# Kernel optimization log

Measured on AMD Instinct MI355X. Metric: run time of the kernel, lower is better.

The kernel has to match this reference:

```python
import jax, jax.numpy as jnp
import numpy as np

B, T, D, H = 128, 256, 64, 512
MISSING = 128.0  # MISSING_VALUE marker from AJ-RNN repo


def _lstm_params(key, in_dim):
    k1, k2 = jax.random.split(key)
    K = jax.random.normal(k1, (in_dim, 4 * H), jnp.float32) * 0.05
    R = jax.random.normal(k2, (H, 4 * H), jnp.float32) * 0.05
    # Keras LSTMCell: zeros bias with unit forget bias (gate order i, f, c, o)
    b = jnp.concatenate([jnp.zeros((H,)), jnp.ones((H,)), jnp.zeros((2 * H,))]).astype(jnp.float32)
    return K, R, b


def setup_inputs() -> dict:
    key = jax.random.key(0)
    ks = jax.random.split(key, 6)
    x = jax.random.normal(ks[0], (B, T, D), jnp.float32)
    miss = jax.random.uniform(ks[1], (B, T, D)) < 0.2
    x = jnp.where(miss, MISSING, x)  # inject missing-value markers
    k0, r0, b0 = _lstm_params(ks[2], D)   # layer 0: input dim D
    k1, r1, b1 = _lstm_params(ks[3], H)   # layer 1: input dim H
    W = jax.random.normal(ks[4], (H, D), jnp.float32) * 0.1  # imputation kernel
    bias = jnp.full((D,), 0.1, jnp.float32)
    return dict(x=x, k0=k0, r0=r0, b0=b0, k1=k1, r1=r1, b1=b1, W=W, bias=bias)


def _lstm_cell(x, h, c, K, R, b):
    z = x @ K + h @ R + b  # [B, 4H]
    i, f, g, o = jnp.split(z, 4, axis=-1)
    i = jax.nn.sigmoid(i)
    f = jax.nn.sigmoid(f)
    g = jnp.tanh(g)
    o = jax.nn.sigmoid(o)
    c_new = f * c + i * g
    h_new = o * jnp.tanh(c_new)
    return h_new, c_new


def reference(x, k0, r0, b0, k1, r1, b1, W, bias):
    xs = jnp.swapaxes(x, 0, 1)          # [T, B, D]
    flags = jnp.arange(T) > 0           # t==0 uses raw input, no imputation

    def step(carry, inp):
        h1, c1, h2, c2 = carry
        x_t, flag = inp
        pred = h2 @ W + bias            # prediction from previous top-layer output
        cur = jnp.where(flag & (x_t == MISSING), pred, x_t)
        h1, c1 = _lstm_cell(cur, h1, c1, k0, r0, b0)
        h2, c2 = _lstm_cell(h1, h2, c2, k1, r1, b1)
        return (h1, c1, h2, c2), h2

    init = tuple(jnp.zeros((B, H), jnp.float32) for _ in range(4))
    _, outs = jax.lax.scan(step, init, (xs, flags))  # outs: [T, B, H]

    # tf.concat(outputs[:-1], axis=1) then reshape [-1, H] == batch-major, time inner
    hidden = jnp.swapaxes(outs[:-1], 0, 1).reshape(-1, H)  # [B*(T-1), H]
    prediction = hidden @ W + bias                          # [B*(T-1), D]
    last_cell = outs[-1]                                    # [B, H]
    return prediction, last_cell
```

## Files before the change

### kernel.cpp

```cpp
#include <hip/hip_runtime.h>
#include <hip/hip_bf16.h>


typedef __bf16        v8bf  __attribute__((ext_vector_type(8)));
typedef float         f32x4 __attribute__((ext_vector_type(4)));
typedef unsigned int  u32x4 __attribute__((ext_vector_type(4)));

constexpr int B_ = 128, T_ = 256, D_ = 64, H_ = 512;

constexpr size_t OFF_WP1 = 0;
constexpr size_t OFF_WP2 = 2359296;
constexpr size_t OFF_WPP = 6553600;
constexpr size_t OFF_H1G = 6619136;
constexpr size_t OFF_H2G = 6750208;
constexpr size_t OFF_FLG = 6881280;

__device__ __forceinline__ v8bf ldv(const __hip_bfloat16* p) {
  return *reinterpret_cast<const v8bf*>(p);
}
__device__ __forceinline__ float sigf(float x) { return 1.0f / (1.0f + __expf(-x)); }
__device__ __forceinline__ float tanhfast(float x) {
  x = fminf(15.0f, fmaxf(-15.0f, x));
  float e = __expf(-2.0f * x);
  return (1.0f - e) / (1.0f + e);
}

__device__ __forceinline__ void st_llc_u16(void* p, unsigned v) {
  asm volatile("global_store_short %0, %1, off sc0 sc1" :: "v"(p), "v"(v) : "memory");
}

__device__ __forceinline__ void ld_llc64(const char* g, u32x4& a, u32x4& b,
                                         u32x4& c, u32x4& d) {
  asm volatile(
      "global_load_dwordx4 %0, %4, off sc0 sc1\n\t"
      "global_load_dwordx4 %1, %4, off offset:16 sc0 sc1\n\t"
      "global_load_dwordx4 %2, %4, off offset:32 sc0 sc1\n\t"
      "global_load_dwordx4 %3, %4, off offset:48 sc0 sc1\n\t"
      "s_waitcnt vmcnt(0)"
      : "=&v"(a), "=&v"(b), "=&v"(c), "=&v"(d)
      : "v"(g)
      : "memory");
}

__device__ __forceinline__ void stage_tile(const __hip_bfloat16* gsrc,
                                           __hip_bfloat16 (*tile)[512], int tid) {
  const int row = tid >> 4;
  const int o0  = (tid & 15) * 64;
  const char* g = (const char*)gsrc + row * 1024 + o0;
  char* lb = (char*)(&tile[row][0]);
  const int sw = (row & 7) << 4;
  u32x4 a, b, c, d;
  ld_llc64(g, a, b, c, d);
  *(u32x4*)(lb + ((o0 +  0) ^ sw)) = a;
  *(u32x4*)(lb + ((o0 + 16) ^ sw)) = b;
  *(u32x4*)(lb + ((o0 + 32) ^ sw)) = c;
  *(u32x4*)(lb + ((o0 + 48) ^ sw)) = d;
}

__global__ __launch_bounds__(256) void pack_weights(
    const float* __restrict__ kp, const float* __restrict__ rp,
    int krows, int ncols, int nkc, int nct, __hip_bfloat16* __restrict__ out) {
  int tid = blockIdx.x * 256 + threadIdx.x;
  int total = nct * nkc * 64;
  if (tid >= total) return;
  int L  = tid & 63;
  int kc = (tid >> 6) % nkc;
  int ct = tid / (64 * nkc);
  int n  = ct * 16 + (L & 15);
  int kb = kc * 32 + (L >> 4) * 8;
  __hip_bfloat16* dst = out + (size_t)tid * 8;
#pragma unroll
  for (int j = 0; j < 8; ++j) {
    int kk = kb + j;
    float v = (kk < krows) ? kp[kk * ncols + n] : rp[(kk - krows) * ncols + n];
    dst[j] = __float2bfloat16(v);
  }
}

__global__ __launch_bounds__(256) void init_state(
    __hip_bfloat16* __restrict__ h1g, __hip_bfloat16* __restrict__ h2g,
    unsigned* __restrict__ flg) {
  int idx = blockIdx.x * 256 + threadIdx.x;
  h1g[idx] = __float2bfloat16(0.0f);
  h2g[idx] = __float2bfloat16(0.0f);
  if (idx < 512) flg[idx] = 0u;
}

__global__ __launch_bounds__(256, 1) void rnn_persist(
    const float* __restrict__ x,
    const __hip_bfloat16* __restrict__ Wp1,
    const __hip_bfloat16* __restrict__ Wp2,
    const __hip_bfloat16* __restrict__ WpP,
    const float* __restrict__ b0,
    const float* __restrict__ b1,
    const float* __restrict__ biasD,
    __hip_bfloat16* __restrict__ h1g,
    __hip_bfloat16* __restrict__ h2g,
    unsigned* __restrict__ flg,
    float* __restrict__ pred_out,
    float* __restrict__ last_out) {

  __shared__ alignas(16) __hip_bfloat16 h1P[16][512];
  __shared__ alignas(16) __hip_bfloat16 h1Q[16][512];
  __shared__ alignas(16) __hip_bfloat16 h2L[16][512];
  __shared__ alignas(16) __hip_bfloat16 curL[16][72];
  __shared__ alignas(16) float predb[16][68];
  __shared__ float zb[4][16][17];

  const int tid = threadIdx.x;
  const int rg = blockIdx.x & 7;
  const int cg = blockIdx.x >> 3;
  const int w  = tid >> 6;
  const int L  = tid & 63;
  const int m  = L & 15;
  const int q  = L >> 4;
  const int row2 = tid >> 4;
  const int col2 = tid & 15;
  const int C  = cg * 16 + col2;
  const int R  = rg * 16 + row2;
  const int sw = (m & 7) << 3;

  v8bf wpp[16], wp1[18], wp2[32];
  {
    const int ct = w * 32 + cg;
#pragma unroll
    for (int kc = 0; kc < 16; ++kc)
      wpp[kc] = ldv(WpP + ((size_t)(w * 16 + kc) * 64 + L) * 8);
#pragma unroll
    for (int kc = 0; kc < 18; ++kc)
      wp1[kc] = ldv(Wp1 + ((size_t)(ct * 18 + kc) * 64 + L) * 8);
#pragma unroll
    for (int kc = 0; kc < 32; ++kc)
      wp2[kc] = ldv(Wp2 + ((size_t)(ct * 32 + kc) * 64 + L) * 8);
  }
  const float b0i = b0[C], b0f = b0[512 + C], b0g = b0[1024 + C], b0o = b0[1536 + C];
  const float b1i = b1[C], b1f = b1[512 + C], b1g = b1[1024 + C], b1o = b1[1536 + C];
  const float bD  = biasD[w * 16 + m];

  float c1v = 0.0f, c2v = 0.0f;

  const size_t rgbase = (size_t)rg * 16 * H_;
  const float* xrow = x + (size_t)R * T_ * D_;
  float* prow = pred_out + (size_t)R * (T_ - 1) * D_;
  unsigned* cnt = flg + rg * 64;
  const int hidx = R * H_ + C;

  stage_tile(h1g + rgbase, h1P, tid);

  for (int t = 0; t < T_; ++t) {
    __hip_bfloat16 (*h1L)[512] = (t & 1) ? h1Q : h1P;
    __hip_bfloat16 (*h1N)[512] = (t & 1) ? h1P : h1Q;

    const int c0 = col2 * 4;
    const float4 xv = *reinterpret_cast<const float4*>(xrow + t * D_ + c0);

    if (t > 0) {
      const unsigned tgt = 64u * (unsigned)t;
      if (tid < 64) {
        while (__hip_atomic_load(cnt, __ATOMIC_RELAXED, __HIP_MEMORY_SCOPE_AGENT) < tgt)
          __builtin_amdgcn_s_sleep(1);
      }
    }
    __syncthreads();

    stage_tile(h2g + rgbase, h2L, tid);
    __syncthreads();

    if (t > 0) {
      f32x4 a0 = {0.f,0.f,0.f,0.f}, a1 = {0.f,0.f,0.f,0.f};
#pragma unroll
      for (int kc = 0; kc < 16; kc += 2) {
        v8bf x0 = ldv(&h2L[m][(kc * 32 + q * 8) ^ sw]);
        v8bf x1 = ldv(&h2L[m][((kc + 1) * 32 + q * 8) ^ sw]);
        a0 = __builtin_amdgcn_mfma_f32_16x16x32_bf16(x0, wpp[kc],     a0, 0, 0, 0);
        a1 = __builtin_amdgcn_mfma_f32_16x16x32_bf16(x1, wpp[kc + 1], a1, 0, 0, 0);
      }
      a0 += a1;
#pragma unroll
      for (int r = 0; r < 4; ++r) predb[q * 4 + r][w * 16 + m] = a0[r] + bD;
    }
    __syncthreads();

    {
      const float4 pv = *reinterpret_cast<const float4*>(&predb[row2][c0]);
      const float xa[4] = {xv.x, xv.y, xv.z, xv.w};
      const float pa[4] = {pv.x, pv.y, pv.z, pv.w};
#pragma unroll
      for (int j = 0; j < 4; ++j) {
        const bool missv = (t > 0) && (xa[j] == 128.0f);
        curL[row2][c0 + j] = __float2bfloat16(missv ? pa[j] : xa[j]);
      }
      if (cg == 0 && t > 0)
        *reinterpret_cast<float4*>(prow + (size_t)(t - 1) * D_ + c0) = pv;
    }
    __syncthreads();

    {
      f32x4 z0 = {0.f,0.f,0.f,0.f}, z1v = {0.f,0.f,0.f,0.f};
      {
        v8bf xa0 = ldv(&curL[m][q * 8]);
        v8bf xa1 = ldv(&curL[m][32 + q * 8]);
        z0  = __builtin_amdgcn_mfma_f32_16x16x32_bf16(xa0, wp1[0], z0, 0, 0, 0);
        z1v = __builtin_amdgcn_mfma_f32_16x16x32_bf16(xa1, wp1[1], z1v, 0, 0, 0);
      }
#pragma unroll
      for (int kc = 2; kc < 18; kc += 2) {
        v8bf xa0 = ldv(&h1L[m][((kc - 2) * 32 + q * 8) ^ sw]);
        v8bf xa1 = ldv(&h1L[m][((kc - 1) * 32 + q * 8) ^ sw]);
        z0  = __builtin_amdgcn_mfma_f32_16x16x32_bf16(xa0, wp1[kc],     z0, 0, 0, 0);
        z1v = __builtin_amdgcn_mfma_f32_16x16x32_bf16(xa1, wp1[kc + 1], z1v, 0, 0, 0);
      }
      z0 += z1v;
#pragma unroll
      for (int r = 0; r < 4; ++r) zb[w][q * 4 + r][m] = z0[r];
    }
    __syncthreads();

    {
      float iv = zb[0][row2][col2] + b0i;
      float fv = zb[1][row2][col2] + b0f;
      float gv = zb[2][row2][col2] + b0g;
      float ov = zb[3][row2][col2] + b0o;
      float ig = sigf(iv), fg = sigf(fv), gg = tanhfast(gv), og = sigf(ov);
      c1v = fg * c1v + ig * gg;
      float hn = og * tanhfast(c1v);
      st_llc_u16(&h1g[hidx], (unsigned)__builtin_bit_cast(unsigned short,
                                                          __float2bfloat16(hn)));
    }

    asm volatile("s_waitcnt vmcnt(0)" ::: "memory");
    __syncthreads();
    if (tid == 0)
      __hip_atomic_fetch_add(cnt, 1u, __ATOMIC_RELAXED, __HIP_MEMORY_SCOPE_AGENT);

    f32x4 zB0 = {0.f,0.f,0.f,0.f}, zB1 = {0.f,0.f,0.f,0.f};
#pragma unroll
    for (int kc = 0; kc < 16; kc += 2) {
      v8bf x0 = ldv(&h2L[m][(kc * 32 + q * 8) ^ sw]);
      v8bf x1 = ldv(&h2L[m][((kc + 1) * 32 + q * 8) ^ sw]);
      zB0 = __builtin_amdgcn_mfma_f32_16x16x32_bf16(x0, wp2[16 + kc],     zB0, 0, 0, 0);
      zB1 = __builtin_amdgcn_mfma_f32_16x16x32_bf16(x1, wp2[16 + kc + 1], zB1, 0, 0, 0);
    }

    {
      const unsigned tgt = 32u * (2u * (unsigned)t + 1u);
      if (tid < 64) {
        while (__hip_atomic_load(cnt, __ATOMIC_RELAXED, __HIP_MEMORY_SCOPE_AGENT) < tgt)
          __builtin_amdgcn_s_sleep(1);
      }
    }
    __syncthreads();
    stage_tile(h1g + rgbase, h1N, tid);
    __syncthreads();

    {
      f32x4 zA0 = {0.f,0.f,0.f,0.f}, zA1 = {0.f,0.f,0.f,0.f};
#pragma unroll
      for (int kc = 0; kc < 16; kc += 2) {
        v8bf x0 = ldv(&h1N[m][(kc * 32 + q * 8) ^ sw]);
        v8bf x1 = ldv(&h1N[m][((kc + 1) * 32 + q * 8) ^ sw]);
        zA0 = __builtin_amdgcn_mfma_f32_16x16x32_bf16(x0, wp2[kc],     zA0, 0, 0, 0);
        zA1 = __builtin_amdgcn_mfma_f32_16x16x32_bf16(x1, wp2[kc + 1], zA1, 0, 0, 0);
      }
      f32x4 zf = (zA0 + zA1) + (zB0 + zB1);
#pragma unroll
      for (int r = 0; r < 4; ++r) zb[w][q * 4 + r][m] = zf[r];
    }
    __syncthreads();

    {
      float iv = zb[0][row2][col2] + b1i;
      float fv = zb[1][row2][col2] + b1f;
      float gv = zb[2][row2][col2] + b1g;
      float ov = zb[3][row2][col2] + b1o;
      float ig = sigf(iv), fg = sigf(fv), gg = tanhfast(gv), og = sigf(ov);
      c2v = fg * c2v + ig * gg;
      float hn = og * tanhfast(c2v);
      if (t == T_ - 1) {
        last_out[hidx] = hn;
      } else {
        st_llc_u16(&h2g[hidx], (unsigned)__builtin_bit_cast(unsigned short,
                                                            __float2bfloat16(hn)));
      }
    }
    if (t == T_ - 1) break;

    asm volatile("s_waitcnt vmcnt(0)" ::: "memory");
    __syncthreads();
    if (tid == 0)
      __hip_atomic_fetch_add(cnt, 1u, __ATOMIC_RELAXED, __HIP_MEMORY_SCOPE_AGENT);
  }
}

extern "C" void kernel_launch(void* const* d_in, const int* in_sizes, int n_in,
                              void* d_out, int out_size, void* d_ws, size_t ws_size,
                              hipStream_t stream) {
  const float* x    = (const float*)d_in[0];
  const float* k0   = (const float*)d_in[1];
  const float* r0   = (const float*)d_in[2];
  const float* b0   = (const float*)d_in[3];
  const float* k1   = (const float*)d_in[4];
  const float* r1   = (const float*)d_in[5];
  const float* b1   = (const float*)d_in[6];
  const float* W    = (const float*)d_in[7];
  const float* bias = (const float*)d_in[8];

  char* ws = (char*)d_ws;
  __hip_bfloat16* Wp1 = (__hip_bfloat16*)(ws + OFF_WP1);
  __hip_bfloat16* Wp2 = (__hip_bfloat16*)(ws + OFF_WP2);
  __hip_bfloat16* WpP = (__hip_bfloat16*)(ws + OFF_WPP);
  __hip_bfloat16* h1g = (__hip_bfloat16*)(ws + OFF_H1G);
  __hip_bfloat16* h2g = (__hip_bfloat16*)(ws + OFF_H2G);
  unsigned*       flg = (unsigned*)(ws + OFF_FLG);

  pack_weights<<<(128 * 18 * 64 + 255) / 256, 256, 0, stream>>>(k0, r0, 64, 2048, 18, 128, Wp1);
  pack_weights<<<(128 * 32 * 64 + 255) / 256, 256, 0, stream>>>(k1, r1, 512, 2048, 32, 128, Wp2);
  pack_weights<<<(4 * 16 * 64 + 255) / 256, 256, 0, stream>>>(W, W, 512, 64, 16, 4, WpP);
  init_state<<<256, 256, 0, stream>>>(h1g, h2g, flg);

  float* outp = (float*)d_out;
  float* last = outp + (size_t)B_ * (T_ - 1) * D_;

  rnn_persist<<<256, 256, 0, stream>>>(x, Wp1, Wp2, WpP, b0, b1, bias,
                                       h1g, h2g, flg, outp, last);
}
```

Measured before the change: 1.551 ms.

## Split K across waves, use per-block flags, and overlap h2 staging with MFMA

Work is repartitioned so each wave handles a K-slice for all four gates instead of one gate over the full K. Partial sums are reduced through shared memory, which adds LDS traffic and an extra barrier per layer. The single atomic counter per row group is replaced by per-block flag stores, which one wave polls with a vector load and __any. The h2 global load is now issued before the recurrent h1 MFMAs so its latency overlaps compute, and layer-2 work on old h2 runs while waiting for the h1 flags. Initial hidden state is zeroed in LDS instead of global memory, so the init kernel shrinks.

Result: slower. 1.715 ms (+10.6%).

```diff
diff --git a/kernel.cpp b/kernel.cpp
--- a/kernel.cpp
+++ b/kernel.cpp
@@ -18,6 +18,9 @@
 __device__ __forceinline__ v8bf ldv(const __hip_bfloat16* p) {
   return *reinterpret_cast<const v8bf*>(p);
 }
+__device__ __forceinline__ f32x4 MF(v8bf a, v8bf b, f32x4 c) {
+  return __builtin_amdgcn_mfma_f32_16x16x32_bf16(a, b, c, 0, 0, 0);
+}
 __device__ __forceinline__ float sigf(float x) { return 1.0f / (1.0f + __expf(-x)); }
 __device__ __forceinline__ float tanhfast(float x) {
   x = fminf(15.0f, fmaxf(-15.0f, x));
@@ -28,33 +31,33 @@
 __device__ __forceinline__ void st_llc_u16(void* p, unsigned v) {
   asm volatile("global_store_short %0, %1, off sc0 sc1" :: "v"(p), "v"(v) : "memory");
 }
-
-__device__ __forceinline__ void ld_llc64(const char* g, u32x4& a, u32x4& b,
-                                         u32x4& c, u32x4& d) {
+__device__ __forceinline__ void st_flag(unsigned* p, unsigned v) {
+  asm volatile("global_store_dword %0, %1, off sc0 sc1" :: "v"(p), "v"(v) : "memory");
+}
+__device__ __forceinline__ void vm0() {
+  asm volatile("s_waitcnt vmcnt(0)" ::: "memory");
+}
+__device__ __forceinline__ void ld_llc64_issue(const char* g, u32x4& a, u32x4& b,
+                                               u32x4& c, u32x4& d) {
   asm volatile(
       "global_load_dwordx4 %0, %4, off sc0 sc1\n\t"
       "global_load_dwordx4 %1, %4, off offset:16 sc0 sc1\n\t"
       "global_load_dwordx4 %2, %4, off offset:32 sc0 sc1\n\t"
-      "global_load_dwordx4 %3, %4, off offset:48 sc0 sc1\n\t"
-      "s_waitcnt vmcnt(0)"
+      "global_load_dwordx4 %3, %4, off offset:48 sc0 sc1"
       : "=&v"(a), "=&v"(b), "=&v"(c), "=&v"(d)
       : "v"(g)
       : "memory");
 }
-
-__device__ __forceinline__ void stage_tile(const __hip_bfloat16* gsrc,
-                                           __hip_bfloat16 (*tile)[512], int tid) {
-  const int row = tid >> 4;
-  const int o0  = (tid & 15) * 64;
-  const char* g = (const char*)gsrc + row * 1024 + o0;
-  char* lb = (char*)(&tile[row][0]);
-  const int sw = (row & 7) << 4;
-  u32x4 a, b, c, d;
-  ld_llc64(g, a, b, c, d);
-  *(u32x4*)(lb + ((o0 +  0) ^ sw)) = a;
-  *(u32x4*)(lb + ((o0 + 16) ^ sw)) = b;
-  *(u32x4*)(lb + ((o0 + 32) ^ sw)) = c;
-  *(u32x4*)(lb + ((o0 + 48) ^ sw)) = d;
+__device__ __forceinline__ void poll_flags(const unsigned* fbase, int lane,
+                                           unsigned tgt) {
+  const unsigned* fp = fbase + (lane & 31);
+  unsigned f;
+  for (;;) {
+    asm volatile("global_load_dword %0, %1, off sc0 sc1\n\ts_waitcnt vmcnt(0)"
+                 : "=v"(f) : "v"(fp) : "memory");
+    if (!__any((int)(f < tgt))) break;
+    __builtin_amdgcn_s_sleep(2);
+  }
 }
 
 __global__ __launch_bounds__(256) void pack_weights(
@@ -77,12 +80,8 @@
   }
 }
 
-__global__ __launch_bounds__(256) void init_state(
-    __hip_bfloat16* __restrict__ h1g, __hip_bfloat16* __restrict__ h2g,
-    unsigned* __restrict__ flg) {
+__global__ __launch_bounds__(256) void init_state(unsigned* __restrict__ flg) {
   int idx = blockIdx.x * 256 + threadIdx.x;
-  h1g[idx] = __float2bfloat16(0.0f);
-  h2g[idx] = __float2bfloat16(0.0f);
   if (idx < 512) flg[idx] = 0u;
 }
 
@@ -104,8 +103,8 @@
   __shared__ alignas(16) __hip_bfloat16 h1Q[16][512];
   __shared__ alignas(16) __hip_bfloat16 h2L[16][512];
   __shared__ alignas(16) __hip_bfloat16 curL[16][72];
-  __shared__ alignas(16) float predb[16][68];
-  __shared__ float zb[4][16][17];
+  __shared__ alignas(16) float predb[4][16][68];
+  __shared__ float zbp[4][4][16][18];
 
   const int tid = threadIdx.x;
   const int rg = blockIdx.x & 7;
@@ -118,162 +117,227 @@
   const int col2 = tid & 15;
   const int C  = cg * 16 + col2;
   const int R  = rg * 16 + row2;
+  const int c0 = col2 * 4;
   const int sw = (m & 7) << 3;
 
-  v8bf wpp[16], wp1[18], wp2[32];
+  const int srow = row2;
+  const int so0  = col2 * 64;
+  const int ssw  = (srow & 7) << 4;
+  const size_t gso = (size_t)srow * 1024 + so0;
+
+  v8bf wpp[4][4], wp1[4][5], wp2[4][8];
   {
-    const int ct = w * 32 + cg;
-#pragma unroll
-    for (int kc = 0; kc < 16; ++kc)
-      wpp[kc] = ldv(WpP + ((size_t)(w * 16 + kc) * 64 + L) * 8);
-#pragma unroll
-    for (int kc = 0; kc < 18; ++kc)
-      wp1[kc] = ldv(Wp1 + ((size_t)(ct * 18 + kc) * 64 + L) * 8);
-#pragma unroll
-    for (int kc = 0; kc < 32; ++kc)
-      wp2[kc] = ldv(Wp2 + ((size_t)(ct * 32 + kc) * 64 + L) * 8);
+#pragma unroll
+    for (int ct = 0; ct < 4; ++ct)
+#pragma unroll
+      for (int k2 = 0; k2 < 4; ++k2)
+        wpp[ct][k2] = ldv(WpP + ((size_t)(ct * 16 + (w * 4 + k2)) * 64 + L) * 8);
+#pragma unroll
+    for (int g = 0; g < 4; ++g) {
+      const size_t ctg1 = (size_t)(g * 32 + cg) * 18;
+      const size_t ctg2 = (size_t)(g * 32 + cg) * 32;
+      if (w < 2) {
+        wp1[g][0] = ldv(Wp1 + ((ctg1 + w) * 64 + L) * 8);
+#pragma unroll
+        for (int i = 1; i <= 4; ++i)
+          wp1[g][i] = ldv(Wp1 + ((ctg1 + (w == 0 ? 1 + i : 5 + i)) * 64 + L) * 8);
+      } else {
+#pragma unroll
+        for (int i = 0; i < 4; ++i)
+          wp1[g][i] = ldv(Wp1 + ((ctg1 + 10 + (w - 2) * 4 + i) * 64 + L) * 8);
+      }
+#pragma unroll
+      for (int k2 = 0; k2 < 8; ++k2)
+        wp2[g][k2] = ldv(Wp2 + ((ctg2 + (w * 8 + k2)) * 64 + L) * 8);
+    }
   }
   const float b0i = b0[C], b0f = b0[512 + C], b0g = b0[1024 + C], b0o = b0[1536 + C];
   const float b1i = b1[C], b1f = b1[512 + C], b1g = b1[1024 + C], b1o = b1[1536 + C];
-  const float bD  = biasD[w * 16 + m];
+  const float4 bD4 = *reinterpret_cast<const float4*>(biasD + c0);
 
   float c1v = 0.0f, c2v = 0.0f;
 
   const size_t rgbase = (size_t)rg * 16 * H_;
   const float* xrow = x + (size_t)R * T_ * D_;
   float* prow = pred_out + (size_t)R * (T_ - 1) * D_;
-  unsigned* cnt = flg + rg * 64;
+  unsigned* fbase = flg + (rg << 6);
   const int hidx = R * H_ + C;
 
-  stage_tile(h1g + rgbase, h1P, tid);
+  {
+    u32x4 zz = {0u, 0u, 0u, 0u};
+    u32x4* p1 = reinterpret_cast<u32x4*>(&h1P[0][0]);
+    u32x4* p2 = reinterpret_cast<u32x4*>(&h2L[0][0]);
+#pragma unroll
+    for (int i = 0; i < 4; ++i) { p1[tid * 4 + i] = zz; p2[tid * 4 + i] = zz; }
+  }
 
   for (int t = 0; t < T_; ++t) {
     __hip_bfloat16 (*h1L)[512] = (t & 1) ? h1Q : h1P;
     __hip_bfloat16 (*h1N)[512] = (t & 1) ? h1P : h1Q;
 
-    const int c0 = col2 * 4;
     const float4 xv = *reinterpret_cast<const float4*>(xrow + t * D_ + c0);
 
+    if (t > 0 && w == 0) poll_flags(fbase, L, 2u * (unsigned)t);
+    __syncthreads();
+
+    u32x4 sa, sb, sc2, sd;
+    if (t > 0)
+      ld_llc64_issue((const char*)(h2g + rgbase) + gso, sa, sb, sc2, sd);
+
+    f32x4 z1a[4] = {{0.f,0.f,0.f,0.f},{0.f,0.f,0.f,0.f},{0.f,0.f,0.f,0.f},{0.f,0.f,0.f,0.f}};
+    if (w < 2) {
+#pragma unroll
+      for (int i = 1; i <= 4; ++i) {
+        const int c = (w == 0 ? 1 + i : 5 + i) - 2;
+        v8bf a = ldv(&h1L[m][(c * 32 + q * 8) ^ sw]);
+#pragma unroll
+        for (int g = 0; g < 4; ++g) z1a[g] = MF(a, wp1[g][i], z1a[g]);
+      }
+    } else {
+#pragma unroll
+      for (int i = 0; i < 4; ++i) {
+        const int c = 8 + (w - 2) * 4 + i;
+        v8bf a = ldv(&h1L[m][(c * 32 + q * 8) ^ sw]);
+#pragma unroll
+        for (int g = 0; g < 4; ++g) z1a[g] = MF(a, wp1[g][i], z1a[g]);
+      }
+    }
+
     if (t > 0) {
-      const unsigned tgt = 64u * (unsigned)t;
-      if (tid < 64) {
-        while (__hip_atomic_load(cnt, __ATOMIC_RELAXED, __HIP_MEMORY_SCOPE_AGENT) < tgt)
-          __builtin_amdgcn_s_sleep(1);
-      }
-    }
-    __syncthreads();
-
-    stage_tile(h2g + rgbase, h2L, tid);
+      vm0();
+      char* lb = (char*)(&h2L[srow][0]);
+      *(u32x4*)(lb + ((so0 +  0) ^ ssw)) = sa;
+      *(u32x4*)(lb + ((so0 + 16) ^ ssw)) = sb;
+      *(u32x4*)(lb + ((so0 + 32) ^ ssw)) = sc2;
+      *(u32x4*)(lb + ((so0 + 48) ^ ssw)) = sd;
+    }
     __syncthreads();
 
     if (t > 0) {
-      f32x4 a0 = {0.f,0.f,0.f,0.f}, a1 = {0.f,0.f,0.f,0.f};
-#pragma unroll
-      for (int kc = 0; kc < 16; kc += 2) {
-        v8bf x0 = ldv(&h2L[m][(kc * 32 + q * 8) ^ sw]);
-        v8bf x1 = ldv(&h2L[m][((kc + 1) * 32 + q * 8) ^ sw]);
-        a0 = __builtin_amdgcn_mfma_f32_16x16x32_bf16(x0, wpp[kc],     a0, 0, 0, 0);
-        a1 = __builtin_amdgcn_mfma_f32_16x16x32_bf16(x1, wpp[kc + 1], a1, 0, 0, 0);
-      }
-      a0 += a1;
-#pragma unroll
-      for (int r = 0; r < 4; ++r) predb[q * 4 + r][w * 16 + m] = a0[r] + bD;
+      f32x4 pa[4] = {{0.f,0.f,0.f,0.f},{0.f,0.f,0.f,0.f},{0.f,0.f,0.f,0.f},{0.f,0.f,0.f,0.f}};
+      v8bf A[4];
+#pragma unroll
+      for (int k2 = 0; k2 < 4; ++k2)
+        A[k2] = ldv(&h2L[m][((w * 4 + k2) * 32 + q * 8) ^ sw]);
+#pragma unroll
+      for (int ct = 0; ct < 4; ++ct)
+#pragma unroll
+        for (int k2 = 0; k2 < 4; ++k2)
+          pa[ct] = MF(A[k2], wpp[ct][k2], pa[ct]);
+#pragma unroll
+      for (int ct = 0; ct < 4; ++ct)
+#pragma unroll
+        for (int r = 0; r < 4; ++r)
+          predb[w][q * 4 + r][ct * 16 + m] = pa[ct][r];
     }
     __syncthreads();
 
     {
-      const float4 pv = *reinterpret_cast<const float4*>(&predb[row2][c0]);
+      float4 pv = {0.f, 0.f, 0.f, 0.f};
+      if (t > 0) {
+#pragma unroll
+        for (int wv = 0; wv < 4; ++wv) {
+          const float4 p = *reinterpret_cast<const float4*>(&predb[wv][row2][c0]);
+          pv.x += p.x; pv.y += p.y; pv.z += p.z; pv.w += p.w;
+        }
+        pv.x += bD4.x; pv.y += bD4.y; pv.z += bD4.z; pv.w += bD4.w;
+      }
       const float xa[4] = {xv.x, xv.y, xv.z, xv.w};
-      const float pa[4] = {pv.x, pv.y, pv.z, pv.w};
+      const float pp[4] = {pv.x, pv.y, pv.z, pv.w};
 #pragma unroll
       for (int j = 0; j < 4; ++j) {
         const bool missv = (t > 0) && (xa[j] == 128.0f);
-        curL[row2][c0 + j] = __float2bfloat16(missv ? pa[j] : xa[j]);
+        curL[row2][c0 + j] = __float2bfloat16(missv ? pp[j] : xa[j]);
       }
       if (cg == 0 && t > 0)
         *reinterpret_cast<float4*>(prow + (size_t)(t - 1) * D_ + c0) = pv;
     }
     __syncthreads();
 
+    if (w < 2) {
+      v8bf a = ldv(&curL[m][w * 32 + q * 8]);
+#pragma unroll
+      for (int g = 0; g < 4; ++g) z1a[g] = MF(a, wp1[g][0], z1a[g]);
+    }
+#pragma unroll
+    for (int g = 0; g < 4; ++g)
+#pragma unroll
+      for (int r = 0; r < 4; ++r)
+        zbp[w][g][q * 4 + r][m] = z1a[g][r];
+    __syncthreads();
+
     {
-      f32x4 z0 = {0.f,0.f,0.f,0.f}, z1v = {0.f,0.f,0.f,0.f};
-      {
-        v8bf xa0 = ldv(&curL[m][q * 8]);
-        v8bf xa1 = ldv(&curL[m][32 + q * 8]);
-        z0  = __builtin_amdgcn_mfma_f32_16x16x32_bf16(xa0, wp1[0], z0, 0, 0, 0);
-        z1v = __builtin_amdgcn_mfma_f32_16x16x32_bf16(xa1, wp1[1], z1v, 0, 0, 0);
-      }
-#pragma unroll
-      for (int kc = 2; kc < 18; kc += 2) {
-        v8bf xa0 = ldv(&h1L[m][((kc - 2) * 32 + q * 8) ^ sw]);
-        v8bf xa1 = ldv(&h1L[m][((kc - 1) * 32 + q * 8) ^ sw]);
-        z0  = __builtin_amdgcn_mfma_f32_16x16x32_bf16(xa0, wp1[kc],     z0, 0, 0, 0);
-        z1v = __builtin_amdgcn_mfma_f32_16x16x32_bf16(xa1, wp1[kc + 1], z1v, 0, 0, 0);
-      }
-      z0 += z1v;
-#pragma unroll
-      for (int r = 0; r < 4; ++r) zb[w][q * 4 + r][m] = z0[r];
-    }
-    __syncthreads();
-
-    {
-      float iv = zb[0][row2][col2] + b0i;
-      float fv = zb[1][row2][col2] + b0f;
-      float gv = zb[2][row2][col2] + b0g;
-      float ov = zb[3][row2][col2] + b0o;
-      float ig = sigf(iv), fg = sigf(fv), gg = tanhfast(gv), og = sigf(ov);
+      float zi = 0.f, zf = 0.f, zg = 0.f, zo = 0.f;
+#pragma unroll
+      for (int wv = 0; wv < 4; ++wv) {
+        zi += zbp[wv][0][row2][col2];
+        zf += zbp[wv][1][row2][col2];
+        zg += zbp[wv][2][row2][col2];
+        zo += zbp[wv][3][row2][col2];
+      }
+      float ig = sigf(zi + b0i), fg = sigf(zf + b0f);
+      float gg = tanhfast(zg + b0g), og = sigf(zo + b0o);
       c1v = fg * c1v + ig * gg;
       float hn = og * tanhfast(c1v);
       st_llc_u16(&h1g[hidx], (unsigned)__builtin_bit_cast(unsigned short,
                                                           __float2bfloat16(hn)));
     }
-
-    asm volatile("s_waitcnt vmcnt(0)" ::: "memory");
-    __syncthreads();
-    if (tid == 0)
-      __hip_atomic_fetch_add(cnt, 1u, __ATOMIC_RELAXED, __HIP_MEMORY_SCOPE_AGENT);
-
-    f32x4 zB0 = {0.f,0.f,0.f,0.f}, zB1 = {0.f,0.f,0.f,0.f};
-#pragma unroll
-    for (int kc = 0; kc < 16; kc += 2) {
-      v8bf x0 = ldv(&h2L[m][(kc * 32 + q * 8) ^ sw]);
-      v8bf x1 = ldv(&h2L[m][((kc + 1) * 32 + q * 8) ^ sw]);
-      zB0 = __builtin_amdgcn_mfma_f32_16x16x32_bf16(x0, wp2[16 + kc],     zB0, 0, 0, 0);
-      zB1 = __builtin_amdgcn_mfma_f32_16x16x32_bf16(x1, wp2[16 + kc + 1], zB1, 0, 0, 0);
-    }
-
+    vm0();
+    __syncthreads();
+    if (tid == 0) st_flag(fbase + cg, 2u * (unsigned)t + 1u);
+
+    f32x4 z2a[4] = {{0.f,0.f,0.f,0.f},{0.f,0.f,0.f,0.f},{0.f,0.f,0.f,0.f},{0.f,0.f,0.f,0.f}};
+    if (w >= 2) {
+#pragma unroll
+      for (int k2 = 0; k2 < 8; ++k2) {
+        const int c = (w - 2) * 8 + k2;
+        v8bf a = ldv(&h2L[m][(c * 32 + q * 8) ^ sw]);
+#pragma unroll
+        for (int g = 0; g < 4; ++g) z2a[g] = MF(a, wp2[g][k2], z2a[g]);
+      }
+    } else if (w == 0) {
+      poll_flags(fbase, L, 2u * (unsigned)t + 1u);
+    }
+    __syncthreads();
+
+    ld_llc64_issue((const char*)(h1g + rgbase) + gso, sa, sb, sc2, sd);
+    vm0();
     {
-      const unsigned tgt = 32u * (2u * (unsigned)t + 1u);
-      if (tid < 64) {
-        while (__hip_atomic_load(cnt, __ATOMIC_RELAXED, __HIP_MEMORY_SCOPE_AGENT) < tgt)
-          __builtin_amdgcn_s_sleep(1);
-      }
-    }
-    __syncthreads();
-    stage_tile(h1g + rgbase, h1N, tid);
+      char* lb = (char*)(&h1N[srow][0]);
+      *(u32x4*)(lb + ((so0 +  0) ^ ssw)) = sa;
+      *(u32x4*)(lb + ((so0 + 16) ^ ssw)) = sb;
+      *(u32x4*)(lb + ((so0 + 32) ^ ssw)) = sc2;
+      *(u32x4*)(lb + ((so0 + 48) ^ ssw)) = sd;
+    }
+    __syncthreads();
+
+    if (w < 2) {
+#pragma unroll
+      for (int k2 = 0; k2 < 8; ++k2) {
+        const int c = w * 8 + k2;
+        v8bf a = ldv(&h1N[m][(c * 32 + q * 8) ^ sw]);
+#pragma unroll
+        for (int g = 0; g < 4; ++g) z2a[g] = MF(a, wp2[g][k2], z2a[g]);
+      }
+    }
+#pragma unroll
+    for (int g = 0; g < 4; ++g)
+#pragma unroll
+      for (int r = 0; r < 4; ++r)
+        zbp[w][g][q * 4 + r][m] = z2a[g][r];
     __syncthreads();
 
     {
-      f32x4 zA0 = {0.f,0.f,0.f,0.f}, zA1 = {0.f,0.f,0.f,0.f};
-#pragma unroll
-      for (int kc = 0; kc < 16; kc += 2) {
-        v8bf x0 = ldv(&h1N[m][(kc * 32 + q * 8) ^ sw]);
-        v8bf x1 = ldv(&h1N[m][((kc + 1) * 32 + q * 8) ^ sw]);
-        zA0 = __builtin_amdgcn_mfma_f32_16x16x32_bf16(x0, wp2[kc],     zA0, 0, 0, 0);
-        zA1 = __builtin_amdgcn_mfma_f32_16x16x32_bf16(x1, wp2[kc + 1], zA1, 0, 0, 0);
-      }
-      f32x4 zf = (zA0 + zA1) + (zB0 + zB1);
-#pragma unroll
-      for (int r = 0; r < 4; ++r) zb[w][q * 4 + r][m] = zf[r];
-    }
-    __syncthreads();
-
-    {
-      float iv = zb[0][row2][col2] + b1i;
-      float fv = zb[1][row2][col2] + b1f;
-      float gv = zb[2][row2][col2] + b1g;
-      float ov = zb[3][row2][col2] + b1o;
-      float ig = sigf(iv), fg = sigf(fv), gg = tanhfast(gv), og = sigf(ov);
+      float zi = 0.f, zf = 0.f, zg = 0.f, zo = 0.f;
+#pragma unroll
+      for (int wv = 0; wv < 4; ++wv) {
+        zi += zbp[wv][0][row2][col2];
+        zf += zbp[wv][1][row2][col2];
+        zg += zbp[wv][2][row2][col2];
+        zo += zbp[wv][3][row2][col2];
+      }
+      float ig = sigf(zi + b1i), fg = sigf(zf + b1f);
+      float gg = tanhfast(zg + b1g), og = sigf(zo + b1o);
       c2v = fg * c2v + ig * gg;
       float hn = og * tanhfast(c2v);
       if (t == T_ - 1) {
@@ -281,14 +345,12 @@
       } else {
         st_llc_u16(&h2g[hidx], (unsigned)__builtin_bit_cast(unsigned short,
                                                             __float2bfloat16(hn)));
+        vm0();
       }
     }
     if (t == T_ - 1) break;
-
-    asm volatile("s_waitcnt vmcnt(0)" ::: "memory");
-    __syncthreads();
-    if (tid == 0)
-      __hip_atomic_fetch_add(cnt, 1u, __ATOMIC_RELAXED, __HIP_MEMORY_SCOPE_AGENT);
+    __syncthreads();
+    if (tid == 0) st_flag(fbase + cg, 2u * (unsigned)t + 2u);
   }
 }
 
@@ -316,7 +378,7 @@
   pack_weights<<<(128 * 18 * 64 + 255) / 256, 256, 0, stream>>>(k0, r0, 64, 2048, 18, 128, Wp1);
   pack_weights<<<(128 * 32 * 64 + 255) / 256, 256, 0, stream>>>(k1, r1, 512, 2048, 32, 128, Wp2);
   pack_weights<<<(4 * 16 * 64 + 255) / 256, 256, 0, stream>>>(W, W, 512, 64, 16, 4, WpP);
-  init_state<<<256, 256, 0, stream>>>(h1g, h2g, flg);
+  init_state<<<2, 256, 0, stream>>>(flg);
 
   float* outp = (float*)d_out;
   float* last = outp + (size_t)B_ * (T_ - 1) * D_;
```

## Replace atomic counter barriers with tagged-value polling and hoist recurrent matmuls

Applied to the files above, without the earlier changes.

Hidden states are now exchanged as 32-bit words that pack a bf16 value with a timestep tag. Consumers poll their own slice until every tag matches, replacing the global atomic counter, the spin-wait, and the fence plus syncthreads before each increment. The h1 recurrent MFMA block is also moved ahead of the h2 wait, overlapping compute with cross-block latency. The cost is twice the exchange traffic, since words are 32 bits, and wider polling loads that are repeated while waiting.

Result: slower. 2.136 ms (+37.8%).

```diff
diff --git a/kernel.cpp b/kernel.cpp
--- a/kernel.cpp
+++ b/kernel.cpp
@@ -11,12 +11,14 @@
 constexpr size_t OFF_WP1 = 0;
 constexpr size_t OFF_WP2 = 2359296;
 constexpr size_t OFF_WPP = 6553600;
-constexpr size_t OFF_H1G = 6619136;
-constexpr size_t OFF_H2G = 6750208;
-constexpr size_t OFF_FLG = 6881280;
+constexpr size_t OFF_H1T = 6619136;
+constexpr size_t OFF_H2T = 6881280;
 
 __device__ __forceinline__ v8bf ldv(const __hip_bfloat16* p) {
   return *reinterpret_cast<const v8bf*>(p);
+}
+__device__ __forceinline__ f32x4 MF(v8bf a, v8bf b, f32x4 c) {
+  return __builtin_amdgcn_mfma_f32_16x16x32_bf16(a, b, c, 0, 0, 0);
 }
 __device__ __forceinline__ float sigf(float x) { return 1.0f / (1.0f + __expf(-x)); }
 __device__ __forceinline__ float tanhfast(float x) {
@@ -25,36 +27,46 @@
   return (1.0f - e) / (1.0f + e);
 }
 
-__device__ __forceinline__ void st_llc_u16(void* p, unsigned v) {
-  asm volatile("global_store_short %0, %1, off sc0 sc1" :: "v"(p), "v"(v) : "memory");
-}
-
-__device__ __forceinline__ void ld_llc64(const char* g, u32x4& a, u32x4& b,
-                                         u32x4& c, u32x4& d) {
-  asm volatile(
-      "global_load_dwordx4 %0, %4, off sc0 sc1\n\t"
-      "global_load_dwordx4 %1, %4, off offset:16 sc0 sc1\n\t"
-      "global_load_dwordx4 %2, %4, off offset:32 sc0 sc1\n\t"
-      "global_load_dwordx4 %3, %4, off offset:48 sc0 sc1\n\t"
-      "s_waitcnt vmcnt(0)"
-      : "=&v"(a), "=&v"(b), "=&v"(c), "=&v"(d)
-      : "v"(g)
-      : "memory");
-}
-
-__device__ __forceinline__ void stage_tile(const __hip_bfloat16* gsrc,
-                                           __hip_bfloat16 (*tile)[512], int tid) {
-  const int row = tid >> 4;
-  const int o0  = (tid & 15) * 64;
-  const char* g = (const char*)gsrc + row * 1024 + o0;
-  char* lb = (char*)(&tile[row][0]);
-  const int sw = (row & 7) << 4;
-  u32x4 a, b, c, d;
-  ld_llc64(g, a, b, c, d);
-  *(u32x4*)(lb + ((o0 +  0) ^ sw)) = a;
-  *(u32x4*)(lb + ((o0 + 16) ^ sw)) = b;
-  *(u32x4*)(lb + ((o0 + 32) ^ sw)) = c;
-  *(u32x4*)(lb + ((o0 + 48) ^ sw)) = d;
+__device__ __forceinline__ void st_llc_u32(void* p, unsigned v) {
+  asm volatile("global_store_dword %0, %1, off sc0 sc1" :: "v"(p), "v"(v) : "memory");
+}
+
+__device__ __forceinline__ void poll_land(const unsigned* g, unsigned tag,
+                                          char* lrow, int so0, int ssw) {
+  u32x4 v0, v1, v2, v3, v4, v5, v6, v7;
+  for (;;) {
+    asm volatile(
+        "global_load_dwordx4 %0, %8, off sc0 sc1\n\t"
+        "global_load_dwordx4 %1, %8, off offset:16 sc0 sc1\n\t"
+        "global_load_dwordx4 %2, %8, off offset:32 sc0 sc1\n\t"
+        "global_load_dwordx4 %3, %8, off offset:48 sc0 sc1\n\t"
+        "global_load_dwordx4 %4, %8, off offset:64 sc0 sc1\n\t"
+        "global_load_dwordx4 %5, %8, off offset:80 sc0 sc1\n\t"
+        "global_load_dwordx4 %6, %8, off offset:96 sc0 sc1\n\t"
+        "global_load_dwordx4 %7, %8, off offset:112 sc0 sc1\n\t"
+        "s_waitcnt vmcnt(0)"
+        : "=&v"(v0), "=&v"(v1), "=&v"(v2), "=&v"(v3),
+          "=&v"(v4), "=&v"(v5), "=&v"(v6), "=&v"(v7)
+        : "v"(g) : "memory");
+    unsigned bad = 0;
+#define CKT(v) bad |= ((v[0] >> 16) ^ tag) | ((v[1] >> 16) ^ tag) | \
+                      ((v[2] >> 16) ^ tag) | ((v[3] >> 16) ^ tag)
+    CKT(v0); CKT(v1); CKT(v2); CKT(v3); CKT(v4); CKT(v5); CKT(v6); CKT(v7);
+#undef CKT
+    if (bad == 0) break;
+    __builtin_amdgcn_s_sleep(1);
+  }
+#define PK(lo, hi) (((lo) & 0xffffu) | ((hi) << 16))
+  u32x4 p;
+  p[0]=PK(v0[0],v0[1]); p[1]=PK(v0[2],v0[3]); p[2]=PK(v1[0],v1[1]); p[3]=PK(v1[2],v1[3]);
+  *(u32x4*)(lrow + ((so0 +  0) ^ ssw)) = p;
+  p[0]=PK(v2[0],v2[1]); p[1]=PK(v2[2],v2[3]); p[2]=PK(v3[0],v3[1]); p[3]=PK(v3[2],v3[3]);
+  *(u32x4*)(lrow + ((so0 + 16) ^ ssw)) = p;
+  p[0]=PK(v4[0],v4[1]); p[1]=PK(v4[2],v4[3]); p[2]=PK(v5[0],v5[1]); p[3]=PK(v5[2],v5[3]);
+  *(u32x4*)(lrow + ((so0 + 32) ^ ssw)) = p;
+  p[0]=PK(v6[0],v6[1]); p[1]=PK(v6[2],v6[3]); p[2]=PK(v7[0],v7[1]); p[3]=PK(v7[2],v7[3]);
+  *(u32x4*)(lrow + ((so0 + 48) ^ ssw)) = p;
+#undef PK
 }
 
 __global__ __launch_bounds__(256) void pack_weights(
@@ -78,12 +90,10 @@
 }
 
 __global__ __launch_bounds__(256) void init_state(
-    __hip_bfloat16* __restrict__ h1g, __hip_bfloat16* __restrict__ h2g,
-    unsigned* __restrict__ flg) {
+    unsigned* __restrict__ h1t, unsigned* __restrict__ h2t) {
   int idx = blockIdx.x * 256 + threadIdx.x;
-  h1g[idx] = __float2bfloat16(0.0f);
-  h2g[idx] = __float2bfloat16(0.0f);
-  if (idx < 512) flg[idx] = 0u;
+  h1t[idx] = 0xFFFF0000u;
+  h2t[idx] = 0xFFFF0000u;
 }
 
 __global__ __launch_bounds__(256, 1) void rnn_persist(
@@ -94,9 +104,8 @@
     const float* __restrict__ b0,
     const float* __restrict__ b1,
     const float* __restrict__ biasD,
-    __hip_bfloat16* __restrict__ h1g,
-    __hip_bfloat16* __restrict__ h2g,
-    unsigned* __restrict__ flg,
+    unsigned* __restrict__ h1t,
+    unsigned* __restrict__ h2t,
     float* __restrict__ pred_out,
     float* __restrict__ last_out) {
 
@@ -118,7 +127,15 @@
   const int col2 = tid & 15;
   const int C  = cg * 16 + col2;
   const int R  = rg * 16 + row2;
+  const int c0 = col2 * 4;
   const int sw = (m & 7) << 3;
+
+  const unsigned* h2slice = h2t + (size_t)rg * 8192 + tid * 32;
+  const unsigned* h1slice = h1t + (size_t)rg * 8192 + tid * 32;
+  const int so0 = (tid & 15) * 64;
+  const int ssw = (row2 & 7) << 4;
+  char* h2row = (char*)&h2L[row2][0];
+  const unsigned gsidx = (unsigned)rg * 8192 + row2 * 512 + cg * 16 + col2;
 
   v8bf wpp[16], wp1[18], wp2[32];
   {
@@ -139,31 +156,35 @@
 
   float c1v = 0.0f, c2v = 0.0f;
 
-  const size_t rgbase = (size_t)rg * 16 * H_;
   const float* xrow = x + (size_t)R * T_ * D_;
   float* prow = pred_out + (size_t)R * (T_ - 1) * D_;
-  unsigned* cnt = flg + rg * 64;
   const int hidx = R * H_ + C;
 
-  stage_tile(h1g + rgbase, h1P, tid);
+  {
+    u32x4 zz = {0u, 0u, 0u, 0u};
+    u32x4* p1 = reinterpret_cast<u32x4*>(&h1P[0][0]);
+    u32x4* p2 = reinterpret_cast<u32x4*>(&h2L[0][0]);
+#pragma unroll
+    for (int i = 0; i < 4; ++i) { p1[tid * 4 + i] = zz; p2[tid * 4 + i] = zz; }
+  }
+  __syncthreads();
 
   for (int t = 0; t < T_; ++t) {
     __hip_bfloat16 (*h1L)[512] = (t & 1) ? h1Q : h1P;
     __hip_bfloat16 (*h1N)[512] = (t & 1) ? h1P : h1Q;
 
-    const int c0 = col2 * 4;
     const float4 xv = *reinterpret_cast<const float4*>(xrow + t * D_ + c0);
 
-    if (t > 0) {
-      const unsigned tgt = 64u * (unsigned)t;
-      if (tid < 64) {
-        while (__hip_atomic_load(cnt, __ATOMIC_RELAXED, __HIP_MEMORY_SCOPE_AGENT) < tgt)
-          __builtin_amdgcn_s_sleep(1);
-      }
-    }
-    __syncthreads();
-
-    stage_tile(h2g + rgbase, h2L, tid);
+    f32x4 z1a = {0.f,0.f,0.f,0.f}, z1b = {0.f,0.f,0.f,0.f};
+#pragma unroll
+    for (int c = 0; c < 16; c += 2) {
+      v8bf a0 = ldv(&h1L[m][(c * 32 + q * 8) ^ sw]);
+      v8bf a1 = ldv(&h1L[m][((c + 1) * 32 + q * 8) ^ sw]);
+      z1a = MF(a0, wp1[2 + c], z1a);
+      z1b = MF(a1, wp1[3 + c], z1b);
+    }
+
+    if (t > 0) poll_land(h2slice, (unsigned)(t - 1), h2row, so0, ssw);
     __syncthreads();
 
     if (t > 0) {
@@ -172,8 +193,8 @@
       for (int kc = 0; kc < 16; kc += 2) {
         v8bf x0 = ldv(&h2L[m][(kc * 32 + q * 8) ^ sw]);
         v8bf x1 = ldv(&h2L[m][((kc + 1) * 32 + q * 8) ^ sw]);
-        a0 = __builtin_amdgcn_mfma_f32_16x16x32_bf16(x0, wpp[kc],     a0, 0, 0, 0);
-        a1 = __builtin_amdgcn_mfma_f32_16x16x32_bf16(x1, wpp[kc + 1], a1, 0, 0, 0);
+        a0 = MF(x0, wpp[kc], a0);
+        a1 = MF(x1, wpp[kc + 1], a1);
       }
       a0 += a1;
 #pragma unroll
@@ -182,7 +203,8 @@
     __syncthreads();
 
     {
-      const float4 pv = *reinterpret_cast<const float4*>(&predb[row2][c0]);
+      float4 pv = {0.f, 0.f, 0.f, 0.f};
+      if (t > 0) pv = *reinterpret_cast<const float4*>(&predb[row2][c0]);
       const float xa[4] = {xv.x, xv.y, xv.z, xv.w};
       const float pa[4] = {pv.x, pv.y, pv.z, pv.w};
 #pragma unroll
@@ -196,23 +218,13 @@
     __syncthreads();
 
     {
-      f32x4 z0 = {0.f,0.f,0.f,0.f}, z1v = {0.f,0.f,0.f,0.f};
-      {
-        v8bf xa0 = ldv(&curL[m][q * 8]);
-        v8bf xa1 = ldv(&curL[m][32 + q * 8]);
-        z0  = __builtin_amdgcn_mfma_f32_16x16x32_bf16(xa0, wp1[0], z0, 0, 0, 0);
-        z1v = __builtin_amdgcn_mfma_f32_16x16x32_bf16(xa1, wp1[1], z1v, 0, 0, 0);
-      }
-#pragma unroll
-      for (int kc = 2; kc < 18; kc += 2) {
-        v8bf xa0 = ldv(&h1L[m][((kc - 2) * 32 + q * 8) ^ sw]);
-        v8bf xa1 = ldv(&h1L[m][((kc - 1) * 32 + q * 8) ^ sw]);
-        z0  = __builtin_amdgcn_mfma_f32_16x16x32_bf16(xa0, wp1[kc],     z0, 0, 0, 0);
-        z1v = __builtin_amdgcn_mfma_f32_16x16x32_bf16(xa1, wp1[kc + 1], z1v, 0, 0, 0);
-      }
-      z0 += z1v;
-#pragma unroll
-      for (int r = 0; r < 4; ++r) zb[w][q * 4 + r][m] = z0[r];
+      v8bf a0 = ldv(&curL[m][q * 8]);
+      v8bf a1 = ldv(&curL[m][32 + q * 8]);
+      z1a = MF(a0, wp1[0], z1a);
+      z1b = MF(a1, wp1[1], z1b);
+      f32x4 zf = z1a + z1b;
+#pragma unroll
+      for (int r = 0; r < 4; ++r) zb[w][q * 4 + r][m] = zf[r];
     }
     __syncthreads();
 
@@ -224,45 +236,31 @@
       float ig = sigf(iv), fg = sigf(fv), gg = tanhfast(gv), og = sigf(ov);
       c1v = fg * c1v + ig * gg;
       float hn = og * tanhfast(c1v);
-      st_llc_u16(&h1g[hidx], (unsigned)__builtin_bit_cast(unsigned short,
-                                                          __float2bfloat16(hn)));
-    }
-
-    asm volatile("s_waitcnt vmcnt(0)" ::: "memory");
-    __syncthreads();
-    if (tid == 0)
-      __hip_atomic_fetch_add(cnt, 1u, __ATOMIC_RELAXED, __HIP_MEMORY_SCOPE_AGENT);
-
-    f32x4 zB0 = {0.f,0.f,0.f,0.f}, zB1 = {0.f,0.f,0.f,0.f};
-#pragma unroll
-    for (int kc = 0; kc < 16; kc += 2) {
-      v8bf x0 = ldv(&h2L[m][(kc * 32 + q * 8) ^ sw]);
-      v8bf x1 = ldv(&h2L[m][((kc + 1) * 32 + q * 8) ^ sw]);
-      zB0 = __builtin_amdgcn_mfma_f32_16x16x32_bf16(x0, wp2[16 + kc],     zB0, 0, 0, 0);
-      zB1 = __builtin_amdgcn_mfma_f32_16x16x32_bf16(x1, wp2[16 + kc + 1], zB1, 0, 0, 0);
-    }
-
-    {
-      const unsigned tgt = 32u * (2u * (unsigned)t + 1u);
-      if (tid < 64) {
-        while (__hip_atomic_load(cnt, __ATOMIC_RELAXED, __HIP_MEMORY_SCOPE_AGENT) < tgt)
-          __builtin_amdgcn_s_sleep(1);
+      unsigned hv = (unsigned)__builtin_bit_cast(unsigned short, __float2bfloat16(hn));
+      st_llc_u32(&h1t[gsidx], ((unsigned)t << 16) | hv);
+    }
+
+    f32x4 z2a = {0.f,0.f,0.f,0.f}, z2b = {0.f,0.f,0.f,0.f};
+#pragma unroll
+    for (int c = 0; c < 16; c += 2) {
+      v8bf a0 = ldv(&h2L[m][(c * 32 + q * 8) ^ sw]);
+      v8bf a1 = ldv(&h2L[m][((c + 1) * 32 + q * 8) ^ sw]);
+      z2a = MF(a0, wp2[16 + c], z2a);
+      z2b = MF(a1, wp2[17 + c], z2b);
+    }
+
+    poll_land(h1slice, (unsigned)t, (char*)&h1N[row2][0], so0, ssw);
+    __syncthreads();
+
+    {
+#pragma unroll
+      for (int c = 0; c < 16; c += 2) {
+        v8bf a0 = ldv(&h1N[m][(c * 32 + q * 8) ^ sw]);
+        v8bf a1 = ldv(&h1N[m][((c + 1) * 32 + q * 8) ^ sw]);
+        z2a = MF(a0, wp2[c], z2a);
+        z2b = MF(a1, wp2[c + 1], z2b);
       }
-    }
-    __syncthreads();
-    stage_tile(h1g + rgbase, h1N, tid);
-    __syncthreads();
-
-    {
-      f32x4 zA0 = {0.f,0.f,0.f,0.f}, zA1 = {0.f,0.f,0.f,0.f};
-#pragma unroll
-      for (int kc = 0; kc < 16; kc += 2) {
-        v8bf x0 = ldv(&h1N[m][(kc * 32 + q * 8) ^ sw]);
-        v8bf x1 = ldv(&h1N[m][((kc + 1) * 32 + q * 8) ^ sw]);
-        zA0 = __builtin_amdgcn_mfma_f32_16x16x32_bf16(x0, wp2[kc],     zA0, 0, 0, 0);
-        zA1 = __builtin_amdgcn_mfma_f32_16x16x32_bf16(x1, wp2[kc + 1], zA1, 0, 0, 0);
-      }
-      f32x4 zf = (zA0 + zA1) + (zB0 + zB1);
+      f32x4 zf = z2a + z2b;
 #pragma unroll
       for (int r = 0; r < 4; ++r) zb[w][q * 4 + r][m] = zf[r];
     }
@@ -279,16 +277,10 @@
       if (t == T_ - 1) {
         last_out[hidx] = hn;
       } else {
-        st_llc_u16(&h2g[hidx], (unsigned)__builtin_bit_cast(unsigned short,
-                                                            __float2bfloat16(hn)));
+        unsigned hv = (unsigned)__builtin_bit_cast(unsigned short, __float2bfloat16(hn));
+        st_llc_u32(&h2t[gsidx], ((unsigned)t << 16) | hv);
       }
     }
-    if (t == T_ - 1) break;
-
-    asm volatile("s_waitcnt vmcnt(0)" ::: "memory");
-    __syncthreads();
-    if (tid == 0)
-      __hip_atomic_fetch_add(cnt, 1u, __ATOMIC_RELAXED, __HIP_MEMORY_SCOPE_AGENT);
   }
 }
 
@@ -309,18 +301,17 @@
   __hip_bfloat16* Wp1 = (__hip_bfloat16*)(ws + OFF_WP1);
   __hip_bfloat16* Wp2 = (__hip_bfloat16*)(ws + OFF_WP2);
   __hip_bfloat16* WpP = (__hip_bfloat16*)(ws + OFF_WPP);
-  __hip_bfloat16* h1g = (__hip_bfloat16*)(ws + OFF_H1G);
-  __hip_bfloat16* h2g = (__hip_bfloat16*)(ws + OFF_H2G);
-  unsigned*       flg = (unsigned*)(ws + OFF_FLG);
+  unsigned*       h1t = (unsigned*)(ws + OFF_H1T);
+  unsigned*       h2t = (unsigned*)(ws + OFF_H2T);
 
   pack_weights<<<(128 * 18 * 64 + 255) / 256, 256, 0, stream>>>(k0, r0, 64, 2048, 18, 128, Wp1);
   pack_weights<<<(128 * 32 * 64 + 255) / 256, 256, 0, stream>>>(k1, r1, 512, 2048, 32, 128, Wp2);
   pack_weights<<<(4 * 16 * 64 + 255) / 256, 256, 0, stream>>>(W, W, 512, 64, 16, 4, WpP);
-  init_state<<<256, 256, 0, stream>>>(h1g, h2g, flg);
+  init_state<<<256, 256, 0, stream>>>(h1t, h2t);
 
   float* outp = (float*)d_out;
   float* last = outp + (size_t)B_ * (T_ - 1) * D_;
 
   rnn_persist<<<256, 256, 0, stream>>>(x, Wp1, Wp2, WpP, b0, b1, bias,
-                                       h1g, h2g, flg, outp, last);
-}
+                                       h1t, h2t, outp, last);
+}
```
